# Kernel optimization log

Measured on AMD Instinct MI355X. Metric: run time of the kernel, lower is better.

Reference implementation:

```python
import jax, jax.numpy as jnp
import numpy as np

BN_EPS = 1e-3  # keras BatchNormalization default epsilon; moving_mean=0, moving_var=1 (init values, inference mode)

def _bn(x, gamma, beta):
    # inference BN with mean=0, var=1: gamma*(x)/sqrt(1+eps) + beta, broadcast over last (channel) axis
    return x * (gamma / jnp.sqrt(1.0 + BN_EPS)) + beta

def _rel_embed(rel, K):
    # reproduces: concat_i rel[K-1-i : 2K-1-i, :] along axis=1 -> emb[a, i] = rel[a - i + K - 1]
    idx = jnp.arange(K)[:, None] - jnp.arange(K)[None, :] + (K - 1)  # [K, K]
    return rel[idx, 0, :]  # [K, K, c]

def _forward(x, w_q, w_k, w_v, q_rel, k_rel, v_rel,
             g_q, b_q, g_k, b_k, g_v, b_v, g_qk, b_qk, g_qr, b_qr,
             g_kr, b_kr, g_sv, b_sv, g_sve, b_sve):
    N, H, W, C = x.shape
    G = g_qk.shape[0]                 # groups = 8
    out_ch = w_v.shape[1]             # 128
    gc = out_ch // G                  # group_ch = 16
    K = H                             # kernel_size == H

    # 1x1 conv transforms (no bias) + BN
    q = _bn(jnp.einsum('bhwc,cd->bhwd', x, w_q), g_q, b_q)  # [N,H,W,out/2]
    k = _bn(jnp.einsum('bhwc,cd->bhwd', x, w_k), g_k, b_k)  # [N,H,W,out/2]
    v = _bn(jnp.einsum('bhwc,cd->bhwd', x, w_v), g_v, b_v)  # [N,H,W,out]

    q_emb = _rel_embed(q_rel, K)  # [K,K,gc/2], used with subscript 'ijc'
    k_emb = _rel_embed(k_rel, K)
    v_emb = _rel_embed(v_rel, K)  # [K,K,gc], used with subscript 'jic'

    q5 = q.reshape(N, H, W, G, gc // 2)
    k5 = k.reshape(N, H, W, G, gc // 2)
    v5 = v.reshape(N, H, W, G, gc)

    qr = jnp.einsum('biwgc,ijc->bijwg', q5, q_emb)   # [N,H,H,W,G]
    qr = _bn(qr, g_qr, b_qr)                         # BN over groups (last axis), same as on (N,-1,W,G)
    kr = jnp.einsum('biwgc,ijc->bijwg', k5, k_emb)
    kr = _bn(kr, g_kr, b_kr)
    kr = jnp.transpose(kr, (0, 2, 1, 3, 4))          # swap i<->j as in source

    qk = jnp.einsum('biwgc,bjwgc->bijwg', q5, k5)    # [N,H,H,W,G]
    qk = _bn(qk, g_qk, b_qk)

    # NOTE: faithful to source: softmax over axis=-2 (the W axis of bijwg)
    sim = jax.nn.softmax(qk + qr + kr, axis=-2)

    sv = jnp.einsum('bijwg,bjwgc->biwgc', sim, v5)   # [N,H,W,G,gc]
    sve = jnp.einsum('bijwg,jic->biwgc', sim, v_emb)

    out = _bn(sv.reshape(N, H, W, out_ch), g_sv, b_sv) + _bn(sve.reshape(N, H, W, out_ch), g_sve, b_sve)
    return out  # [N,H,W,out_ch]


def setup_inputs() -> dict:
    key = jax.random.key(0)
    ks = jax.random.split(key, 32)
    N, H, W, C = 32, 56, 56, 128
    OUT, G, K = 128, 8, 56
    gc = OUT // G  # 16

    x = jax.random.normal(ks[0], (N, H, W, C), jnp.float32)

    w_q = jax.random.normal(ks[1], (C, OUT // 2), jnp.float32) * np.sqrt(1.0 / C * gc)
    w_k = jax.random.normal(ks[2], (C, OUT // 2), jnp.float32) * np.sqrt(1.0 / C)
    w_v = jax.random.normal(ks[3], (C, OUT), jnp.float32) * np.sqrt(1.0 / C)

    q_rel = jax.random.normal(ks[4], (2 * K - 1, 1, gc // 2), jnp.float32) * np.sqrt(1.0 / (OUT // 2))
    k_rel = jax.random.normal(ks[5], (2 * K - 1, 1, gc // 2), jnp.float32) * np.sqrt(1.0 / (OUT // 2))
    v_rel = jax.random.normal(ks[6], (2 * K - 1, 1, gc), jnp.float32) * np.sqrt(1.0 / OUT)

    def bn_params(k1, k2, c):
        gamma = jax.random.uniform(k1, (c,), jnp.float32, 0.5, 1.5)
        beta = 0.1 * jax.random.normal(k2, (c,), jnp.float32)
        return gamma, beta

    g_q, b_q = bn_params(ks[7], ks[8], OUT // 2)
    g_k, b_k = bn_params(ks[9], ks[10], OUT // 2)
    g_v, b_v = bn_params(ks[11], ks[12], OUT)
    g_qk, b_qk = bn_params(ks[13], ks[14], G)
    g_qr, b_qr = bn_params(ks[15], ks[16], G)
    g_kr, b_kr = bn_params(ks[17], ks[18], G)
    g_sv, b_sv = bn_params(ks[19], ks[20], OUT)
    g_sve, b_sve = bn_params(ks[21], ks[22], OUT)

    return dict(x=x, w_q=w_q, w_k=w_k, w_v=w_v, q_rel=q_rel, k_rel=k_rel, v_rel=v_rel,
                g_q=g_q, b_q=b_q, g_k=g_k, b_k=b_k, g_v=g_v, b_v=b_v,
                g_qk=g_qk, b_qk=b_qk, g_qr=g_qr, b_qr=b_qr, g_kr=g_kr, b_kr=b_kr,
                g_sv=g_sv, b_sv=b_sv, g_sve=g_sve, b_sve=b_sve)


def reference(x, w_q, w_k, w_v, q_rel, k_rel, v_rel,
              g_q, b_q, g_k, b_k, g_v, b_v, g_qk, b_qk, g_qr, b_qr,
              g_kr, b_kr, g_sv, b_sv, g_sve, b_sve):
    return _forward(x, w_q, w_k, w_v, q_rel, k_rel, v_rel,
                    g_q, b_q, g_k, b_k, g_v, b_v, g_qk, b_qk, g_qr, b_qr,
                    g_kr, b_kr, g_sv, b_sv, g_sve, b_sve)
```

## Files before the change

### kernel.cpp

```cpp
#include <hip/hip_runtime.h>
#include <math.h>


typedef _Float16 f16;
typedef _Float16 f16x2 __attribute__((ext_vector_type(2)));
typedef _Float16 f16x4 __attribute__((ext_vector_type(4)));
typedef _Float16 f16x8 __attribute__((ext_vector_type(8)));
typedef float    f32x4 __attribute__((ext_vector_type(4)));
typedef unsigned int u32;
typedef unsigned int u32x2 __attribute__((ext_vector_type(2)));

static constexpr int NB    = 32;
static constexpr int HH    = 56;
static constexpr int CIN   = 128;
static constexpr int GG    = 8;
static constexpr int PLANE = HH * HH;
static constexpr int MT    = 112;
static constexpr int NBLK  = 28;

__global__ __launch_bounds__(256) void prep_kernel(
    const float* __restrict__ wq, const float* __restrict__ wk,
    const float* __restrict__ wv, f16* __restrict__ wt)
{
    const int id = blockIdx.x * 256 + threadIdx.x;
    const int d = id >> 4, kc = id & 15;
    const float* src; int stride, dl;
    if (d < 64)       { src = wq; stride = 64;  dl = d; }
    else if (d < 128) { src = wk; stride = 64;  dl = d - 64; }
    else              { src = wv; stride = 128; dl = d - 128; }
    f16x8 v;
    #pragma unroll
    for (int kk = 0; kk < 8; ++kk)
        v[kk] = (f16)src[(kc * 8 + kk) * stride + dl];
    *(f16x8*)&wt[d * 128 + kc * 8] = v;
}

__global__ __launch_bounds__(256, 2) void qkv_kernel(
    const float* __restrict__ x, const f16* __restrict__ wt,
    const float* __restrict__ gq, const float* __restrict__ bq,
    const float* __restrict__ gk, const float* __restrict__ bk,
    const float* __restrict__ gv, const float* __restrict__ bv,
    f16* __restrict__ qt, f16* __restrict__ kt, f16* __restrict__ vt2)
{
    __shared__ f16 lds_a[MT * 136];
    __shared__ f16 lds_b[128 * 136];

    const int t    = threadIdx.x;
    const int nh   = blockIdx.y;
    const int b    = blockIdx.x / NBLK;
    const int B28  = blockIdx.x - b * NBLK;
    const int rem0 = B28 * MT;
    const size_t m0 = (size_t)b * PLANE + rem0;

    {
        const float4* xs = (const float4*)(x + m0 * CIN);
        #pragma unroll
        for (int it = 0; it < 14; ++it) {
            const int f = it * 256 + t;
            const int r = f >> 5, c = f & 31;
            const float4 v = xs[f];
            f16x4 p; p.x = (f16)v.x; p.y = (f16)v.y; p.z = (f16)v.z; p.w = (f16)v.w;
            *(f16x4*)&lds_a[r * 136 + c * 4] = p;
        }
    }
    #pragma unroll
    for (int it = 0; it < 8; ++it) {
        const int f = it * 256 + t;
        const int n = f >> 4, kc = f & 15;
        *(f16x8*)&lds_b[n * 136 + kc * 8] =
            *(const f16x8*)&wt[(size_t)(nh * 128 + n) * 128 + kc * 8];
    }
    __syncthreads();

    const int lane = t & 63, wid = t >> 6;
    const int wn0 = wid * 32;
    const int ra = lane & 15, qd = lane >> 4;

    f32x4 acc[7][2];
    #pragma unroll
    for (int mt = 0; mt < 7; ++mt)
        #pragma unroll
        for (int nt = 0; nt < 2; ++nt)
            acc[mt][nt] = (f32x4){0.f, 0.f, 0.f, 0.f};

    #pragma unroll
    for (int ks = 0; ks < 4; ++ks) {
        f16x8 af[7], bf[2];
        #pragma unroll
        for (int mt = 0; mt < 7; ++mt)
            af[mt] = *(const f16x8*)&lds_a[(mt * 16 + ra) * 136 + ks * 32 + qd * 8];
        #pragma unroll
        for (int nt = 0; nt < 2; ++nt)
            bf[nt] = *(const f16x8*)&lds_b[(wn0 + nt * 16 + ra) * 136 + ks * 32 + qd * 8];
        #pragma unroll
        for (int mt = 0; mt < 7; ++mt)
            #pragma unroll
            for (int nt = 0; nt < 2; ++nt)
                acc[mt][nt] = __builtin_amdgcn_mfma_f32_16x16x32_f16(
                    af[mt], bf[nt], acc[mt][nt], 0, 0, 0);
    }
    __syncthreads();

    f16* lds_c = lds_a;
    const float inv = 1.0f / sqrtf(1.001f);
    #pragma unroll
    for (int nt = 0; nt < 2; ++nt) {
        const int d  = wn0 + nt * 16 + ra;
        const int dg = nh * 128 + d;
        float scale, shift;
        if (dg < 64)       { scale = gq[dg] * inv;        shift = bq[dg]; }
        else if (dg < 128) { scale = gk[dg - 64] * inv;   shift = bk[dg - 64]; }
        else               { scale = gv[dg - 128] * inv;  shift = bv[dg - 128]; }
        #pragma unroll
        for (int mt = 0; mt < 7; ++mt)
            #pragma unroll
            for (int rg = 0; rg < 4; ++rg) {
                const int m = mt * 16 + qd * 4 + rg;
                lds_c[m * 136 + d] = (f16)fmaf(acc[mt][nt][rg], scale, shift);
            }
    }
    __syncthreads();

    if (nh == 0) {
        const int rl = t & 31, gs2 = t >> 5;
        #pragma unroll
        for (int it = 0; it < 4; ++it) {
            const int rem = it * 32 + rl;
            if (rem < MT) {
                #pragma unroll
                for (int half = 0; half < 2; ++half) {
                    const int gslot = half * 8 + gs2;
                    const f16x8 v = *(const f16x8*)&lds_c[rem * 136 + gslot * 8];
                    f16* dst = (gslot < 8) ? qt : kt;
                    const int g = gslot & 7;
                    *(f16x8*)&dst[((size_t)(b * GG + g) * PLANE + rem0 + rem) * 8] = v;
                }
            }
        }
    } else {
        const int cq = t & 3, w8 = (t >> 2) & 7, g = t >> 5;
        #pragma unroll
        for (int it = 0; it < 7; ++it) {
            const int w = it * 8 + w8;
            const int doff = g * 16 + cq * 4;
            const u32x2 a  = *(const u32x2*)&lds_c[w * 136 + doff];
            const u32x2 bb = *(const u32x2*)&lds_c[(56 + w) * 136 + doff];
            uint4 o;
            o.x = __builtin_amdgcn_perm(a.x, bb.x, 0x01000504u);
            o.y = __builtin_amdgcn_perm(a.x, bb.x, 0x03020706u);
            o.z = __builtin_amdgcn_perm(a.y, bb.y, 0x01000504u);
            o.w = __builtin_amdgcn_perm(a.y, bb.y, 0x03020706u);
            const size_t base =
                (((size_t)(b * GG + g) * NBLK + B28) * HH + w) * 32 + cq * 8;
            *(uint4*)&vt2[base] = o;
        }
    }
}

__global__ __launch_bounds__(256) void attn_kernel(
    const f16* __restrict__ qt, const f16* __restrict__ kt, const f16* __restrict__ vt2,
    const float* __restrict__ q_rel, const float* __restrict__ k_rel, const float* __restrict__ v_rel,
    const float* __restrict__ g_qk, const float* __restrict__ b_qk,
    const float* __restrict__ g_qr, const float* __restrict__ b_qr,
    const float* __restrict__ g_kr, const float* __restrict__ b_kr,
    const float* __restrict__ g_sv, const float* __restrict__ b_sv,
    const float* __restrict__ g_sve, const float* __restrict__ b_sve,
    float* __restrict__ out)
{
    const int i = blockIdx.x;
    const int g = blockIdx.y;
    const int b = blockIdx.z;
    const int t = threadIdx.x;

    __shared__ float s32[56][57];
    __shared__ f16 s16[56 * 58];
    __shared__ f16 qi[56 * 8];
    __shared__ f16 qe[56 * 8];
    __shared__ f16 ke[56 * 8];
    __shared__ f16 ve2[28 * 32];

    const float inv = 1.0f / sqrtf(1.001f);
    const int bg = (b * GG + g) * PLANE;

    if (t < 56)
        *(f16x8*)&qi[t * 8] = *(const f16x8*)&qt[(size_t)(bg + i * HH + t) * 8];
    for (int idx = t; idx < 448; idx += 256) {
        const int j = idx >> 3, c = idx & 7;
        qe[idx] = (f16)q_rel[(i - j + 55) * 8 + c];
        ke[idx] = (f16)k_rel[(j - i + 55) * 8 + c];
    }
    for (int idx = t; idx < 896; idx += 256) {
        const int J = idx >> 5, r = idx & 31, c = r >> 1, jb = r & 1;
        ve2[idx] = (f16)v_rel[(2 * J + jb - i + 55) * 16 + c];
    }
    const float sqk = g_qk[g] * inv, bqk = b_qk[g];
    const float sqr = g_qr[g] * inv, bqr = b_qr[g];
    const float skr = g_kr[g] * inv, bkr = b_kr[g];
    __syncthreads();

    {
        const int wv = t >> 6, lane = t & 63;
        const int wc = (lane < 56) ? lane : 55;
        const f16x8 qv = *(const f16x8*)&qi[wc * 8];
        for (int jj = 0; jj < 14; ++jj) {
            const int j = wv * 14 + jj;
            const f16x8 kv = *(const f16x8*)&kt[(size_t)(bg + j * HH + wc) * 8];
            const f16x8 ev = *(const f16x8*)&qe[j * 8];
            const f16x8 fv = *(const f16x8*)&ke[j * 8];
            float qk = 0.f, qr = 0.f, kr = 0.f;
            #pragma unroll
            for (int c = 0; c < 4; ++c) {
                const f16x2 kk = ((const f16x2*)&kv)[c];
                const f16x2 qq = ((const f16x2*)&qv)[c];
                qk = __builtin_amdgcn_fdot2(qq, kk, qk, false);
                qr = __builtin_amdgcn_fdot2(qq, ((const f16x2*)&ev)[c], qr, false);
                kr = __builtin_amdgcn_fdot2(kk, ((const f16x2*)&fv)[c], kr, false);
            }
            const float s = fmaf(sqk, qk, bqk) + fmaf(sqr, qr, bqr) + fmaf(skr, kr, bkr);
            if (lane < 56) s32[j][lane] = s;
        }
    }
    __syncthreads();

    if (t < 224) {
        const int j = t >> 2, q = t & 3;
        const int w0 = q * 14;
        float v[14];
        #pragma unroll
        for (int wi = 0; wi < 14; ++wi) v[wi] = s32[j][w0 + wi];
        float mx = v[0];
        #pragma unroll
        for (int wi = 1; wi < 14; ++wi) mx = fmaxf(mx, v[wi]);
        mx = fmaxf(mx, __shfl_xor(mx, 1));
        mx = fmaxf(mx, __shfl_xor(mx, 2));
        float e[14];
        float sum = 0.f;
        #pragma unroll
        for (int wi = 0; wi < 14; ++wi) { e[wi] = __expf(v[wi] - mx); sum += e[wi]; }
        sum += __shfl_xor(sum, 1);
        sum += __shfl_xor(sum, 2);
        const float rs = __builtin_amdgcn_rcpf(sum);
        #pragma unroll
        for (int wi = 0; wi < 14; ++wi)
            s16[(w0 + wi) * 58 + j] = (f16)(e[wi] * rs);
    }
    __syncthreads();

    if (t < 224) {
        const int w = t >> 2, cq = t & 3;
        const f16* vp = vt2 + ((size_t)(b * GG + g) * NBLK * HH + w) * 32 + cq * 8;
        float sv[4] = {0.f, 0.f, 0.f, 0.f};
        float se[4] = {0.f, 0.f, 0.f, 0.f};
        #pragma unroll 2
        for (int J = 0; J < 28; J += 2) {
            const f16x4 pp4 = *(const f16x4*)&s16[w * 58 + 2 * J];
            #pragma unroll
            for (int u = 0; u < 2; ++u) {
                const f16x2 pp = ((const f16x2*)&pp4)[u];
                const f16x8 vl = *(const f16x8*)(vp + (size_t)(J + u) * (HH * 32));
                const f16x8 el = *(const f16x8*)&ve2[(J + u) * 32 + cq * 8];
                #pragma unroll
                for (int c = 0; c < 4; ++c) {
                    sv[c] = __builtin_amdgcn_fdot2(pp, ((const f16x2*)&vl)[c], sv[c], false);
                    se[c] = __builtin_amdgcn_fdot2(pp, ((const f16x2*)&el)[c], se[c], false);
                }
            }
        }
        const int ch = g * 16 + cq * 4;
        const float4 gsv  = *(const float4*)(g_sv + ch);
        const float4 bsv  = *(const float4*)(b_sv + ch);
        const float4 gsve = *(const float4*)(g_sve + ch);
        const float4 bsve = *(const float4*)(b_sve + ch);
        float4 o;
        o.x = fmaf(gsv.x * inv, sv[0], bsv.x) + fmaf(gsve.x * inv, se[0], bsve.x);
        o.y = fmaf(gsv.y * inv, sv[1], bsv.y) + fmaf(gsve.y * inv, se[1], bsve.y);
        o.z = fmaf(gsv.z * inv, sv[2], bsv.z) + fmaf(gsve.z * inv, se[2], bsve.z);
        o.w = fmaf(gsv.w * inv, sv[3], bsv.w) + fmaf(gsve.w * inv, se[3], bsve.w);
        *(float4*)(out + ((size_t)(b * HH + i) * HH + w) * 128 + ch) = o;
    }
}

extern "C" void kernel_launch(void* const* d_in, const int* in_sizes, int n_in,
                              void* d_out, int out_size, void* d_ws, size_t ws_size,
                              hipStream_t stream)
{
    const float* x     = (const float*)d_in[0];
    const float* w_q   = (const float*)d_in[1];
    const float* w_k   = (const float*)d_in[2];
    const float* w_v   = (const float*)d_in[3];
    const float* q_rel = (const float*)d_in[4];
    const float* k_rel = (const float*)d_in[5];
    const float* v_rel = (const float*)d_in[6];
    const float* g_q   = (const float*)d_in[7];
    const float* b_q   = (const float*)d_in[8];
    const float* g_k   = (const float*)d_in[9];
    const float* b_k   = (const float*)d_in[10];
    const float* g_v   = (const float*)d_in[11];
    const float* b_v   = (const float*)d_in[12];
    const float* g_qk  = (const float*)d_in[13];
    const float* b_qk  = (const float*)d_in[14];
    const float* g_qr  = (const float*)d_in[15];
    const float* b_qr  = (const float*)d_in[16];
    const float* g_kr  = (const float*)d_in[17];
    const float* b_kr  = (const float*)d_in[18];
    const float* g_sv  = (const float*)d_in[19];
    const float* b_sv  = (const float*)d_in[20];
    const float* g_sve = (const float*)d_in[21];
    const float* b_sve = (const float*)d_in[22];
    float* out = (float*)d_out;

    f16* wt  = (f16*)d_ws;
    f16* qt  = wt + 32768;
    f16* kt  = qt + (size_t)NB * GG * PLANE * 8;
    f16* vt2 = kt + (size_t)NB * GG * PLANE * 8;

    prep_kernel<<<16, 256, 0, stream>>>(w_q, w_k, w_v, wt);

    qkv_kernel<<<dim3((NB * PLANE) / MT, 2), 256, 0, stream>>>(
        x, wt, g_q, b_q, g_k, b_k, g_v, b_v, qt, kt, vt2);

    attn_kernel<<<dim3(56, 8, 32), 256, 0, stream>>>(
        qt, kt, vt2, q_rel, k_rel, v_rel,
        g_qk, b_qk, g_qr, b_qr, g_kr, b_kr, g_sv, b_sv, g_sve, b_sve, out);
}
```

Measured before the change: 257.8 us.

## Process two query rows per attention block and fold BN scales into operands

Each attention block now handles two adjacent rows i, so every loaded key and value vector serves both rows. The grid is halved and shared buffers are doubled. The BN scales for qk, qr, kr and sve are folded into the q, relative-embedding and v_emb operands, which merges the separate dot-product accumulators into one and drops per-element fma work. The softmax output aliases the score buffer, which adds an extra barrier. Pre-scaling in fp16 slightly changes rounding and divides by gamma.

```diff
diff --git a/kernel.cpp b/kernel.cpp
--- a/kernel.cpp
+++ b/kernel.cpp
@@ -167,116 +167,169 @@
     const float* __restrict__ g_sve, const float* __restrict__ b_sve,
     float* __restrict__ out)
 {
-    const int i = blockIdx.x;
-    const int g = blockIdx.y;
-    const int b = blockIdx.z;
-    const int t = threadIdx.x;
-
-    __shared__ float s32[56][57];
-    __shared__ f16 s16[56 * 58];
-    __shared__ f16 qi[56 * 8];
-    __shared__ f16 qe[56 * 8];
-    __shared__ f16 ke[56 * 8];
-    __shared__ f16 ve2[28 * 32];
+    const int i0 = blockIdx.x * 2;
+    const int g  = blockIdx.y;
+    const int b  = blockIdx.z;
+    const int t  = threadIdx.x;
+
+    __shared__ float s32[2][56][57];
+    __shared__ f16 qi [2][56 * 8];
+    __shared__ f16 qe [2][56 * 8];
+    __shared__ f16 ke [2][56 * 8];
+    __shared__ f16 ve2[2][28 * 32];
+    f16* const s16 = (f16*)&s32[0][0][0];
 
     const float inv = 1.0f / sqrtf(1.001f);
     const int bg = (b * GG + g) * PLANE;
 
-    if (t < 56)
-        *(f16x8*)&qi[t * 8] = *(const f16x8*)&qt[(size_t)(bg + i * HH + t) * 8];
-    for (int idx = t; idx < 448; idx += 256) {
-        const int j = idx >> 3, c = idx & 7;
-        qe[idx] = (f16)q_rel[(i - j + 55) * 8 + c];
-        ke[idx] = (f16)k_rel[(j - i + 55) * 8 + c];
+    const float sqk = g_qk[g] * inv;
+    const float sqr = g_qr[g] * inv;
+    const float skr = g_kr[g] * inv;
+    const float r_qr = sqr / sqk;
+    const float bias = b_qk[g] + b_qr[g] + b_kr[g];
+
+    if (t < 112) {
+        const int ii = (t >= 56) ? 1 : 0;
+        const int w  = t - ii * 56;
+        f16x8 v = *(const f16x8*)&qt[(size_t)(bg + (i0 + ii) * HH + w) * 8];
+        #pragma unroll
+        for (int c = 0; c < 8; ++c) v[c] = (f16)((float)v[c] * sqk);
+        *(f16x8*)&qi[ii][w * 8] = v;
     }
     for (int idx = t; idx < 896; idx += 256) {
-        const int J = idx >> 5, r = idx & 31, c = r >> 1, jb = r & 1;
-        ve2[idx] = (f16)v_rel[(2 * J + jb - i + 55) * 16 + c];
-    }
-    const float sqk = g_qk[g] * inv, bqk = b_qk[g];
-    const float sqr = g_qr[g] * inv, bqr = b_qr[g];
-    const float skr = g_kr[g] * inv, bkr = b_kr[g];
+        const int ii = (idx >= 448) ? 1 : 0;
+        const int r  = idx - ii * 448;
+        const int j = r >> 3, c = r & 7;
+        const int iv = i0 + ii;
+        qe[ii][r] = (f16)(r_qr * q_rel[(iv - j + 55) * 8 + c]);
+        ke[ii][r] = (f16)(skr  * k_rel[(j - iv + 55) * 8 + c]);
+    }
+    for (int idx = t; idx < 1792; idx += 256) {
+        const int ii = (idx >= 896) ? 1 : 0;
+        const int rr = idx - ii * 896;
+        const int J = rr >> 5, r = rr & 31, c = r >> 1, jb = r & 1;
+        const int ch = g * 16 + c;
+        const float ratio = g_sve[ch] / g_sv[ch];
+        ve2[ii][rr] = (f16)(ratio * v_rel[(2 * J + jb - (i0 + ii) + 55) * 16 + c]);
+    }
     __syncthreads();
 
     {
         const int wv = t >> 6, lane = t & 63;
         const int wc = (lane < 56) ? lane : 55;
-        const f16x8 qv = *(const f16x8*)&qi[wc * 8];
+        const f16x8 qv0 = *(const f16x8*)&qi[0][wc * 8];
+        const f16x8 qv1 = *(const f16x8*)&qi[1][wc * 8];
+        const f16* kbase = kt + (size_t)(bg + wv * 14 * HH + wc) * 8;
+        #pragma unroll
         for (int jj = 0; jj < 14; ++jj) {
             const int j = wv * 14 + jj;
-            const f16x8 kv = *(const f16x8*)&kt[(size_t)(bg + j * HH + wc) * 8];
-            const f16x8 ev = *(const f16x8*)&qe[j * 8];
-            const f16x8 fv = *(const f16x8*)&ke[j * 8];
-            float qk = 0.f, qr = 0.f, kr = 0.f;
-            #pragma unroll
-            for (int c = 0; c < 4; ++c) {
-                const f16x2 kk = ((const f16x2*)&kv)[c];
-                const f16x2 qq = ((const f16x2*)&qv)[c];
-                qk = __builtin_amdgcn_fdot2(qq, kk, qk, false);
-                qr = __builtin_amdgcn_fdot2(qq, ((const f16x2*)&ev)[c], qr, false);
-                kr = __builtin_amdgcn_fdot2(kk, ((const f16x2*)&fv)[c], kr, false);
+            const f16x8 kv = *(const f16x8*)(kbase + (size_t)jj * (HH * 8));
+            #pragma unroll
+            for (int ii = 0; ii < 2; ++ii) {
+                const f16x8 qv = ii ? qv1 : qv0;
+                const f16x8 ev = *(const f16x8*)&qe[ii][j * 8];
+                const f16x8 fv = *(const f16x8*)&ke[ii][j * 8];
+                float s = bias;
+                #pragma unroll
+                for (int c = 0; c < 4; ++c) {
+                    const f16x2 kk = ((const f16x2*)&kv)[c];
+                    const f16x2 qq = ((const f16x2*)&qv)[c];
+                    s = __builtin_amdgcn_fdot2(qq, kk, s, false);
+                    s = __builtin_amdgcn_fdot2(qq, ((const f16x2*)&ev)[c], s, false);
+                    s = __builtin_amdgcn_fdot2(kk, ((const f16x2*)&fv)[c], s, false);
+                }
+                s32[ii][j][wc] = s;
             }
-            const float s = fmaf(sqk, qk, bqk) + fmaf(sqr, qr, bqr) + fmaf(skr, kr, bkr);
-            if (lane < 56) s32[j][lane] = s;
-        }
-    }
-    __syncthreads();
-
-    if (t < 224) {
-        const int j = t >> 2, q = t & 3;
-        const int w0 = q * 14;
-        float v[14];
-        #pragma unroll
-        for (int wi = 0; wi < 14; ++wi) v[wi] = s32[j][w0 + wi];
-        float mx = v[0];
-        #pragma unroll
-        for (int wi = 1; wi < 14; ++wi) mx = fmaxf(mx, v[wi]);
-        mx = fmaxf(mx, __shfl_xor(mx, 1));
-        mx = fmaxf(mx, __shfl_xor(mx, 2));
-        float e[14];
-        float sum = 0.f;
-        #pragma unroll
-        for (int wi = 0; wi < 14; ++wi) { e[wi] = __expf(v[wi] - mx); sum += e[wi]; }
-        sum += __shfl_xor(sum, 1);
-        sum += __shfl_xor(sum, 2);
-        const float rs = __builtin_amdgcn_rcpf(sum);
-        #pragma unroll
-        for (int wi = 0; wi < 14; ++wi)
-            s16[(w0 + wi) * 58 + j] = (f16)(e[wi] * rs);
+        }
+    }
+    __syncthreads();
+
+    float e[2][14];
+    float rs[2];
+    #pragma unroll
+    for (int uu = 0; uu < 2; ++uu) {
+        const int u = t + uu * 256;
+        if (u < 448) {
+            const int ii = (u >= 224) ? 1 : 0;
+            const int r  = u - ii * 224;
+            const int j = r >> 2, q = r & 3, w0 = q * 14;
+            float v[14];
+            #pragma unroll
+            for (int wi = 0; wi < 14; ++wi) v[wi] = s32[ii][j][w0 + wi];
+            float mx = v[0];
+            #pragma unroll
+            for (int wi = 1; wi < 14; ++wi) mx = fmaxf(mx, v[wi]);
+            mx = fmaxf(mx, __shfl_xor(mx, 1));
+            mx = fmaxf(mx, __shfl_xor(mx, 2));
+            float sum = 0.f;
+            #pragma unroll
+            for (int wi = 0; wi < 14; ++wi) { e[uu][wi] = __expf(v[wi] - mx); sum += e[uu][wi]; }
+            sum += __shfl_xor(sum, 1);
+            sum += __shfl_xor(sum, 2);
+            rs[uu] = __builtin_amdgcn_rcpf(sum);
+        }
+    }
+    __syncthreads();
+    #pragma unroll
+    for (int uu = 0; uu < 2; ++uu) {
+        const int u = t + uu * 256;
+        if (u < 448) {
+            const int ii = (u >= 224) ? 1 : 0;
+            const int r  = u - ii * 224;
+            const int j = r >> 2, q = r & 3, w0 = q * 14;
+            f16* sbase = s16 + ii * (56 * 58);
+            #pragma unroll
+            for (int wi = 0; wi < 14; ++wi)
+                sbase[(w0 + wi) * 58 + j] = (f16)(e[uu][wi] * rs[uu]);
+        }
     }
     __syncthreads();
 
     if (t < 224) {
         const int w = t >> 2, cq = t & 3;
-        const f16* vp = vt2 + ((size_t)(b * GG + g) * NBLK * HH + w) * 32 + cq * 8;
-        float sv[4] = {0.f, 0.f, 0.f, 0.f};
-        float se[4] = {0.f, 0.f, 0.f, 0.f};
-        #pragma unroll 2
-        for (int J = 0; J < 28; J += 2) {
-            const f16x4 pp4 = *(const f16x4*)&s16[w * 58 + 2 * J];
+        const f16* vp  = vt2 + ((size_t)(b * GG + g) * NBLK * HH + w) * 32 + cq * 8;
+        const f16* sp0 = s16 + w * 58;
+        const f16* sp1 = s16 + 56 * 58 + w * 58;
+        const f16* ep0 = &ve2[0][cq * 8];
+        const f16* ep1 = &ve2[1][cq * 8];
+        float acc[2][4] = {{0.f, 0.f, 0.f, 0.f}, {0.f, 0.f, 0.f, 0.f}};
+        #pragma unroll
+        for (int Jp = 0; Jp < 14; ++Jp) {
+            const f16x4 p0 = *(const f16x4*)(sp0 + 4 * Jp);
+            const f16x4 p1 = *(const f16x4*)(sp1 + 4 * Jp);
             #pragma unroll
             for (int u = 0; u < 2; ++u) {
-                const f16x2 pp = ((const f16x2*)&pp4)[u];
-                const f16x8 vl = *(const f16x8*)(vp + (size_t)(J + u) * (HH * 32));
-                const f16x8 el = *(const f16x8*)&ve2[(J + u) * 32 + cq * 8];
+                const int j2 = 2 * Jp + u;
+                const f16x8 vl = *(const f16x8*)(vp + (size_t)j2 * (HH * 32));
+                const f16x8 el0 = *(const f16x8*)(ep0 + j2 * 32);
+                const f16x8 el1 = *(const f16x8*)(ep1 + j2 * 32);
+                const f16x2 pp[2] = { ((const f16x2*)&p0)[u], ((const f16x2*)&p1)[u] };
                 #pragma unroll
-                for (int c = 0; c < 4; ++c) {
-                    sv[c] = __builtin_amdgcn_fdot2(pp, ((const f16x2*)&vl)[c], sv[c], false);
-                    se[c] = __builtin_amdgcn_fdot2(pp, ((const f16x2*)&el)[c], se[c], false);
+                for (int ii = 0; ii < 2; ++ii) {
+                    const f16x8 el = ii ? el1 : el0;
+                    #pragma unroll
+                    for (int c = 0; c < 4; ++c) {
+                        acc[ii][c] = __builtin_amdgcn_fdot2(
+                            pp[ii], ((const f16x2*)&el)[c], acc[ii][c], false);
+                        acc[ii][c] = __builtin_amdgcn_fdot2(
+                            pp[ii], ((const f16x2*)&vl)[c], acc[ii][c], false);
+                    }
                 }
             }
         }
         const int ch = g * 16 + cq * 4;
         const float4 gsv  = *(const float4*)(g_sv + ch);
         const float4 bsv  = *(const float4*)(b_sv + ch);
-        const float4 gsve = *(const float4*)(g_sve + ch);
         const float4 bsve = *(const float4*)(b_sve + ch);
-        float4 o;
-        o.x = fmaf(gsv.x * inv, sv[0], bsv.x) + fmaf(gsve.x * inv, se[0], bsve.x);
-        o.y = fmaf(gsv.y * inv, sv[1], bsv.y) + fmaf(gsve.y * inv, se[1], bsve.y);
-        o.z = fmaf(gsv.z * inv, sv[2], bsv.z) + fmaf(gsve.z * inv, se[2], bsve.z);
-        o.w = fmaf(gsv.w * inv, sv[3], bsv.w) + fmaf(gsve.w * inv, se[3], bsve.w);
-        *(float4*)(out + ((size_t)(b * HH + i) * HH + w) * 128 + ch) = o;
+        #pragma unroll
+        for (int ii = 0; ii < 2; ++ii) {
+            float4 o;
+            o.x = fmaf(gsv.x * inv, acc[ii][0], bsv.x + bsve.x);
+            o.y = fmaf(gsv.y * inv, acc[ii][1], bsv.y + bsve.y);
+            o.z = fmaf(gsv.z * inv, acc[ii][2], bsv.z + bsve.z);
+            o.w = fmaf(gsv.w * inv, acc[ii][3], bsv.w + bsve.w);
+            *(float4*)(out + ((size_t)(b * HH + i0 + ii) * HH + w) * 128 + ch) = o;
+        }
     }
 }
 
@@ -319,7 +372,7 @@
     qkv_kernel<<<dim3((NB * PLANE) / MT, 2), 256, 0, stream>>>(
         x, wt, g_q, b_q, g_k, b_k, g_v, b_v, qt, kt, vt2);
 
-    attn_kernel<<<dim3(56, 8, 32), 256, 0, stream>>>(
+    attn_kernel<<<dim3(28, 8, 32), 256, 0, stream>>>(
         qt, kt, vt2, q_rel, k_rel, v_rel,
         g_qk, b_qk, g_qr, b_qr, g_kr, b_kr, g_sv, b_sv, g_sve, b_sve, out);
 }
```

New measurement: 296.6 us. 1.15x slower.

## Fold BN scales into operands and compute relative-value term with MFMA

Applied to the files above, without the earlier changes.

Pre-scales q and the relative embeddings by the BN ratios so the three logit dot products accumulate into one sum with a single combined bias. The sve (relative value embedding) contraction becomes a 16x16x32 MFMA over a transposed, zero-padded embedding tile, and the sv contraction is restructured so each lane handles one channel across four w rows. The output BN for sv and sve is merged into one fma via a g_sve/g_sv ratio folded into the embedding. This trades some fp16 precision, plus division by g_sv, for fewer ALU ops and removes the per-thread vector loads of the embedding. The global V loads shrink from 16-byte to 4-byte per lane, which may hurt memory efficiency.

```diff
diff --git a/kernel.cpp b/kernel.cpp
--- a/kernel.cpp
+++ b/kernel.cpp
@@ -173,51 +173,62 @@
     const int t = threadIdx.x;
 
     __shared__ float s32[56][57];
-    __shared__ f16 s16[56 * 58];
-    __shared__ f16 qi[56 * 8];
-    __shared__ f16 qe[56 * 8];
-    __shared__ f16 ke[56 * 8];
-    __shared__ f16 ve2[28 * 32];
+    __shared__ __attribute__((aligned(16))) f16 s16[64 * 72];
+    __shared__ __attribute__((aligned(16))) f16 qi[56 * 8];
+    __shared__ __attribute__((aligned(16))) f16 qe[56 * 8];
+    __shared__ __attribute__((aligned(16))) f16 ke[56 * 8];
+    __shared__ __attribute__((aligned(16))) f16 veT[16 * 72];
 
     const float inv = 1.0f / sqrtf(1.001f);
     const int bg = (b * GG + g) * PLANE;
 
-    if (t < 56)
-        *(f16x8*)&qi[t * 8] = *(const f16x8*)&qt[(size_t)(bg + i * HH + t) * 8];
+    const float sqk  = g_qk[g] * inv;
+    const float r_qr = (g_qr[g] * inv) / sqk;
+    const float skr  = g_kr[g] * inv;
+    const float bias = b_qk[g] + b_qr[g] + b_kr[g];
+
+    if (t < 56) {
+        f16x8 v = *(const f16x8*)&qt[(size_t)(bg + i * HH + t) * 8];
+        #pragma unroll
+        for (int c = 0; c < 8; ++c) v[c] = (f16)((float)v[c] * sqk);
+        *(f16x8*)&qi[t * 8] = v;
+    }
     for (int idx = t; idx < 448; idx += 256) {
         const int j = idx >> 3, c = idx & 7;
-        qe[idx] = (f16)q_rel[(i - j + 55) * 8 + c];
-        ke[idx] = (f16)k_rel[(j - i + 55) * 8 + c];
-    }
-    for (int idx = t; idx < 896; idx += 256) {
-        const int J = idx >> 5, r = idx & 31, c = r >> 1, jb = r & 1;
-        ve2[idx] = (f16)v_rel[(2 * J + jb - i + 55) * 16 + c];
-    }
-    const float sqk = g_qk[g] * inv, bqk = b_qk[g];
-    const float sqr = g_qr[g] * inv, bqr = b_qr[g];
-    const float skr = g_kr[g] * inv, bkr = b_kr[g];
+        qe[idx] = (f16)(r_qr * q_rel[(i - j + 55) * 8 + c]);
+        ke[idx] = (f16)(skr  * k_rel[(j - i + 55) * 8 + c]);
+    }
+    for (int idx = t; idx < 1024; idx += 256) {
+        const int c = idx >> 6, j = idx & 63;
+        const int ch = g * 16 + c;
+        const float ratio = g_sve[ch] / g_sv[ch];
+        veT[c * 72 + j] = (j < 56)
+            ? (f16)(ratio * v_rel[(j - i + 55) * 16 + c]) : (f16)0.f;
+    }
+    for (int idx = t; idx < 2304; idx += 256)
+        ((u32*)s16)[idx] = 0u;
     __syncthreads();
 
     {
         const int wv = t >> 6, lane = t & 63;
         const int wc = (lane < 56) ? lane : 55;
         const f16x8 qv = *(const f16x8*)&qi[wc * 8];
+        const f16* kbase = kt + (size_t)(bg + wv * 14 * HH + wc) * 8;
         for (int jj = 0; jj < 14; ++jj) {
             const int j = wv * 14 + jj;
-            const f16x8 kv = *(const f16x8*)&kt[(size_t)(bg + j * HH + wc) * 8];
+            const f16x8 kv = *(const f16x8*)(kbase + (size_t)jj * (HH * 8));
             const f16x8 ev = *(const f16x8*)&qe[j * 8];
             const f16x8 fv = *(const f16x8*)&ke[j * 8];
-            float qk = 0.f, qr = 0.f, kr = 0.f;
+            float s = bias;
             #pragma unroll
             for (int c = 0; c < 4; ++c) {
                 const f16x2 kk = ((const f16x2*)&kv)[c];
                 const f16x2 qq = ((const f16x2*)&qv)[c];
-                qk = __builtin_amdgcn_fdot2(qq, kk, qk, false);
-                qr = __builtin_amdgcn_fdot2(qq, ((const f16x2*)&ev)[c], qr, false);
-                kr = __builtin_amdgcn_fdot2(kk, ((const f16x2*)&fv)[c], kr, false);
-            }
-            const float s = fmaf(sqk, qk, bqk) + fmaf(sqr, qr, bqr) + fmaf(skr, kr, bkr);
-            if (lane < 56) s32[j][lane] = s;
+                s = __builtin_amdgcn_fdot2(qq, kk, s, false);
+                s = __builtin_amdgcn_fdot2(qq, ((const f16x2*)&ev)[c], s, false);
+                s = __builtin_amdgcn_fdot2(kk, ((const f16x2*)&fv)[c], s, false);
+            }
+            s32[j][wc] = s;
         }
     }
     __syncthreads();
@@ -242,41 +253,57 @@
         const float rs = __builtin_amdgcn_rcpf(sum);
         #pragma unroll
         for (int wi = 0; wi < 14; ++wi)
-            s16[(w0 + wi) * 58 + j] = (f16)(e[wi] * rs);
-    }
-    __syncthreads();
-
-    if (t < 224) {
-        const int w = t >> 2, cq = t & 3;
-        const f16* vp = vt2 + ((size_t)(b * GG + g) * NBLK * HH + w) * 32 + cq * 8;
-        float sv[4] = {0.f, 0.f, 0.f, 0.f};
-        float se[4] = {0.f, 0.f, 0.f, 0.f};
-        #pragma unroll 2
-        for (int J = 0; J < 28; J += 2) {
-            const f16x4 pp4 = *(const f16x4*)&s16[w * 58 + 2 * J];
-            #pragma unroll
-            for (int u = 0; u < 2; ++u) {
-                const f16x2 pp = ((const f16x2*)&pp4)[u];
-                const f16x8 vl = *(const f16x8*)(vp + (size_t)(J + u) * (HH * 32));
-                const f16x8 el = *(const f16x8*)&ve2[(J + u) * 32 + cq * 8];
+            s16[(w0 + wi) * 72 + j] = (f16)(e[wi] * rs);
+    }
+    __syncthreads();
+
+    {
+        const int lane = t & 63, wid = t >> 6;
+        const int c = lane & 15, qd = lane >> 4;
+
+        f32x4 eacc = (f32x4){0.f, 0.f, 0.f, 0.f};
+        {
+            const f16* arow = &s16[(wid * 16 + c) * 72];
+            const f16* brow = &veT[c * 72];
+            #pragma unroll
+            for (int ks = 0; ks < 2; ++ks) {
+                const f16x8 af = *(const f16x8*)&arow[ks * 32 + qd * 8];
+                const f16x8 bf = *(const f16x8*)&brow[ks * 32 + qd * 8];
+                eacc = __builtin_amdgcn_mfma_f32_16x16x32_f16(af, bf, eacc, 0, 0, 0);
+            }
+        }
+
+        const int wb = wid * 16 + qd * 4;
+        float acc[4] = {0.f, 0.f, 0.f, 0.f};
+        {
+            const f16* sp[4]; const f16* vp[4];
+            #pragma unroll
+            for (int rg = 0; rg < 4; ++rg) {
+                const int wc = (wb + rg < 56) ? (wb + rg) : 55;
+                sp[rg] = &s16[wc * 72];
+                vp[rg] = vt2 + (size_t)(b * GG + g) * (NBLK * HH * 32) + wc * 32 + c * 2;
+            }
+            #pragma unroll 4
+            for (int J = 0; J < 28; ++J) {
                 #pragma unroll
-                for (int c = 0; c < 4; ++c) {
-                    sv[c] = __builtin_amdgcn_fdot2(pp, ((const f16x2*)&vl)[c], sv[c], false);
-                    se[c] = __builtin_amdgcn_fdot2(pp, ((const f16x2*)&el)[c], se[c], false);
+                for (int rg = 0; rg < 4; ++rg) {
+                    const f16x2 pp = *(const f16x2*)(sp[rg] + 2 * J);
+                    const f16x2 vv = *(const f16x2*)(vp[rg] + (size_t)J * (HH * 32));
+                    acc[rg] = __builtin_amdgcn_fdot2(pp, vv, acc[rg], false);
                 }
             }
         }
-        const int ch = g * 16 + cq * 4;
-        const float4 gsv  = *(const float4*)(g_sv + ch);
-        const float4 bsv  = *(const float4*)(b_sv + ch);
-        const float4 gsve = *(const float4*)(g_sve + ch);
-        const float4 bsve = *(const float4*)(b_sve + ch);
-        float4 o;
-        o.x = fmaf(gsv.x * inv, sv[0], bsv.x) + fmaf(gsve.x * inv, se[0], bsve.x);
-        o.y = fmaf(gsv.y * inv, sv[1], bsv.y) + fmaf(gsve.y * inv, se[1], bsve.y);
-        o.z = fmaf(gsv.z * inv, sv[2], bsv.z) + fmaf(gsve.z * inv, se[2], bsve.z);
-        o.w = fmaf(gsv.w * inv, sv[3], bsv.w) + fmaf(gsve.w * inv, se[3], bsve.w);
-        *(float4*)(out + ((size_t)(b * HH + i) * HH + w) * 128 + ch) = o;
+
+        const int ch = g * 16 + c;
+        const float gs = g_sv[ch] * inv;
+        const float bb = b_sv[ch] + b_sve[ch];
+        #pragma unroll
+        for (int rg = 0; rg < 4; ++rg) {
+            const int w = wb + rg;
+            if (w < 56)
+                out[((size_t)(b * HH + i) * HH + w) * 128 + ch] =
+                    fmaf(gs, acc[rg] + eacc[rg], bb);
+        }
     }
 }
 
```

Result: slower. 280.8 us (+8.9%).

## Fold BN scales into f16 operands, alias softmax buffer, raise occupancy

Applied to the files above, without the earlier changes.

Folds the qk, qr and kr BatchNorm scales and biases into pre-scaled q and embedding operands, so the three dot products accumulate into one register with a single combined bias. The f16 softmax output buffer now aliases the fp32 score buffer, with an extra barrier between reading and writing it, which cuts LDS per block. Launch bounds request 8 blocks per SM, and the k load loop is unrolled with a precomputed base pointer. This trades some f16 precision (pre-scaled q, ratio-scaled embeddings) and one extra barrier for lower LDS and register pressure and higher occupancy.

```diff
diff --git a/kernel.cpp b/kernel.cpp
--- a/kernel.cpp
+++ b/kernel.cpp
@@ -157,7 +157,7 @@
     }
 }
 
-__global__ __launch_bounds__(256) void attn_kernel(
+__global__ __launch_bounds__(256, 8) void attn_kernel(
     const f16* __restrict__ qt, const f16* __restrict__ kt, const f16* __restrict__ vt2,
     const float* __restrict__ q_rel, const float* __restrict__ k_rel, const float* __restrict__ v_rel,
     const float* __restrict__ g_qk, const float* __restrict__ b_qk,
@@ -173,76 +173,90 @@
     const int t = threadIdx.x;
 
     __shared__ float s32[56][57];
-    __shared__ f16 s16[56 * 58];
-    __shared__ f16 qi[56 * 8];
-    __shared__ f16 qe[56 * 8];
-    __shared__ f16 ke[56 * 8];
-    __shared__ f16 ve2[28 * 32];
+    __shared__ __attribute__((aligned(16))) f16 qi[56 * 8];
+    __shared__ __attribute__((aligned(16))) f16 qe[56 * 8];
+    __shared__ __attribute__((aligned(16))) f16 ke[56 * 8];
+    __shared__ __attribute__((aligned(16))) f16 ve2[28 * 32];
+    f16* const s16 = (f16*)&s32[0][0];
 
     const float inv = 1.0f / sqrtf(1.001f);
     const int bg = (b * GG + g) * PLANE;
 
-    if (t < 56)
-        *(f16x8*)&qi[t * 8] = *(const f16x8*)&qt[(size_t)(bg + i * HH + t) * 8];
+    const float sqk  = g_qk[g] * inv;
+    const float r_qr = (g_qr[g] * inv) / sqk;
+    const float skr  = g_kr[g] * inv;
+    const float bias = b_qk[g] + b_qr[g] + b_kr[g];
+
+    if (t < 56) {
+        f16x8 v = *(const f16x8*)&qt[(size_t)(bg + i * HH + t) * 8];
+        #pragma unroll
+        for (int c = 0; c < 8; ++c) v[c] = (f16)((float)v[c] * sqk);
+        *(f16x8*)&qi[t * 8] = v;
+    }
     for (int idx = t; idx < 448; idx += 256) {
         const int j = idx >> 3, c = idx & 7;
-        qe[idx] = (f16)q_rel[(i - j + 55) * 8 + c];
-        ke[idx] = (f16)k_rel[(j - i + 55) * 8 + c];
+        qe[idx] = (f16)(r_qr * q_rel[(i - j + 55) * 8 + c]);
+        ke[idx] = (f16)(skr  * k_rel[(j - i + 55) * 8 + c]);
     }
     for (int idx = t; idx < 896; idx += 256) {
         const int J = idx >> 5, r = idx & 31, c = r >> 1, jb = r & 1;
         ve2[idx] = (f16)v_rel[(2 * J + jb - i + 55) * 16 + c];
     }
-    const float sqk = g_qk[g] * inv, bqk = b_qk[g];
-    const float sqr = g_qr[g] * inv, bqr = b_qr[g];
-    const float skr = g_kr[g] * inv, bkr = b_kr[g];
     __syncthreads();
 
     {
         const int wv = t >> 6, lane = t & 63;
         const int wc = (lane < 56) ? lane : 55;
         const f16x8 qv = *(const f16x8*)&qi[wc * 8];
+        const f16* kbase = kt + (size_t)(bg + wv * 14 * HH + wc) * 8;
+        #pragma unroll 2
         for (int jj = 0; jj < 14; ++jj) {
             const int j = wv * 14 + jj;
-            const f16x8 kv = *(const f16x8*)&kt[(size_t)(bg + j * HH + wc) * 8];
+            const f16x8 kv = *(const f16x8*)(kbase + (size_t)jj * (HH * 8));
             const f16x8 ev = *(const f16x8*)&qe[j * 8];
             const f16x8 fv = *(const f16x8*)&ke[j * 8];
-            float qk = 0.f, qr = 0.f, kr = 0.f;
+            float s = bias;
             #pragma unroll
             for (int c = 0; c < 4; ++c) {
                 const f16x2 kk = ((const f16x2*)&kv)[c];
                 const f16x2 qq = ((const f16x2*)&qv)[c];
-                qk = __builtin_amdgcn_fdot2(qq, kk, qk, false);
-                qr = __builtin_amdgcn_fdot2(qq, ((const f16x2*)&ev)[c], qr, false);
-                kr = __builtin_amdgcn_fdot2(kk, ((const f16x2*)&fv)[c], kr, false);
+                s = __builtin_amdgcn_fdot2(qq, kk, s, false);
+                s = __builtin_amdgcn_fdot2(qq, ((const f16x2*)&ev)[c], s, false);
+                s = __builtin_amdgcn_fdot2(kk, ((const f16x2*)&fv)[c], s, false);
             }
-            const float s = fmaf(sqk, qk, bqk) + fmaf(sqr, qr, bqr) + fmaf(skr, kr, bkr);
-            if (lane < 56) s32[j][lane] = s;
-        }
-    }
-    __syncthreads();
-
-    if (t < 224) {
-        const int j = t >> 2, q = t & 3;
-        const int w0 = q * 14;
-        float v[14];
-        #pragma unroll
-        for (int wi = 0; wi < 14; ++wi) v[wi] = s32[j][w0 + wi];
-        float mx = v[0];
-        #pragma unroll
-        for (int wi = 1; wi < 14; ++wi) mx = fmaxf(mx, v[wi]);
-        mx = fmaxf(mx, __shfl_xor(mx, 1));
-        mx = fmaxf(mx, __shfl_xor(mx, 2));
+            s32[j][wc] = s;
+        }
+    }
+    __syncthreads();
+
+    {
+        const bool act = (t < 224);
+        int j = 0, w0 = 0;
         float e[14];
-        float sum = 0.f;
-        #pragma unroll
-        for (int wi = 0; wi < 14; ++wi) { e[wi] = __expf(v[wi] - mx); sum += e[wi]; }
-        sum += __shfl_xor(sum, 1);
-        sum += __shfl_xor(sum, 2);
-        const float rs = __builtin_amdgcn_rcpf(sum);
-        #pragma unroll
-        for (int wi = 0; wi < 14; ++wi)
-            s16[(w0 + wi) * 58 + j] = (f16)(e[wi] * rs);
+        float rs = 0.f;
+        if (act) {
+            j = t >> 2; w0 = (t & 3) * 14;
+            float v[14];
+            #pragma unroll
+            for (int wi = 0; wi < 14; ++wi) v[wi] = s32[j][w0 + wi];
+            float mx = v[0];
+            #pragma unroll
+            for (int wi = 1; wi < 14; ++wi) mx = fmaxf(mx, v[wi]);
+            mx = fmaxf(mx, __shfl_xor(mx, 1));
+            mx = fmaxf(mx, __shfl_xor(mx, 2));
+            float sum = 0.f;
+            #pragma unroll
+            for (int wi = 0; wi < 14; ++wi) { e[wi] = __expf(v[wi] - mx); sum += e[wi]; }
+            sum += __shfl_xor(sum, 1);
+            sum += __shfl_xor(sum, 2);
+            rs = __builtin_amdgcn_rcpf(sum);
+        }
+        __syncthreads();
+        if (act) {
+            #pragma unroll
+            for (int wi = 0; wi < 14; ++wi)
+                s16[(w0 + wi) * 58 + j] = (f16)(e[wi] * rs);
+        }
     }
     __syncthreads();
 
```

Result: slower. 284.0 us (+10.2%).
